# Optimization experiments

Hardware: AMD Instinct MI355X
Metric: run time of the kernel (lower is better)

## Reference

```python
import jax, jax.numpy as jnp
import numpy as np

HDIM = 1024
N_CLASSES = 50257
CUTOFFS = [2000, 10000, N_CLASSES]  # shortlist=2000, clusters: [2000,10000), [10000,50257)
DIV = 4.0
HEAD_SIZE = CUTOFFS[0] + 2  # shortlist + 2 cluster logits


def setup_inputs() -> dict:
    key = jax.random.key(0)
    ks = jax.random.split(key, 12)
    B, S, K = 8, 512, 256
    N = B * K
    hsz0 = int(HDIM // (DIV ** 1))  # 256
    hsz1 = int(HDIM // (DIV ** 2))  # 64
    osz0 = CUTOFFS[1] - CUTOFFS[0]  # 8000
    osz1 = CUTOFFS[2] - CUTOFFS[1]  # 40257
    w = 0.02
    return {
        "targets": jax.random.randint(ks[0], (N,), 0, N_CLASSES),
        "last_hidden_states": jax.random.normal(ks[1], (B, S, HDIM), dtype=jnp.float32),
        "cls_tokens_batch": jax.random.normal(ks[2], (B, HDIM), dtype=jnp.float32),
        "idx": jax.random.randint(ks[3], (B, K), 0, S),
        "head_W": jax.random.normal(ks[4], (HEAD_SIZE, HDIM), dtype=jnp.float32) * w,
        "head_b": jnp.zeros((HEAD_SIZE,), dtype=jnp.float32),
        "proj0_W": jax.random.normal(ks[5], (hsz0, HDIM), dtype=jnp.float32) * w,
        "out0_W": jax.random.normal(ks[6], (osz0, hsz0), dtype=jnp.float32) * w,
        "proj1_W": jax.random.normal(ks[7], (hsz1, HDIM), dtype=jnp.float32) * w,
        "out1_W": jax.random.normal(ks[8], (osz1, hsz1), dtype=jnp.float32) * w,
    }


def reference(targets, last_hidden_states, cls_tokens_batch, idx,
              head_W, head_b, proj0_W, out0_W, proj1_W, out1_W):
    # Gather context token embeddings: [B, K, H] -> [N, H]
    B, S, H = last_hidden_states.shape
    x = last_hidden_states[jnp.arange(B)[:, None], idx].reshape(-1, H)
    N = x.shape[0]
    c0, c1 = CUTOFFS[0], CUTOFFS[1]

    # Head: shortlist logits + per-cluster routing logits, [N, c0+2]
    head_logprob = jax.nn.log_softmax(x @ head_W.T + head_b, axis=-1)
    # Tail clusters: low-rank projection then output GEMM + log-softmax
    lp0 = jax.nn.log_softmax((x @ proj0_W.T) @ out0_W.T, axis=-1)  # [N, 8000]
    lp1 = jax.nn.log_softmax((x @ proj1_W.T) @ out1_W.T, axis=-1)  # [N, 40257]

    n = jnp.arange(N)
    t = targets
    short = head_logprob[n, jnp.clip(t, 0, c0 - 1)]
    mid = head_logprob[:, c0] + lp0[n, jnp.clip(t - c0, 0, lp0.shape[1] - 1)]
    high = head_logprob[:, c0 + 1] + lp1[n, jnp.clip(t - c1, 0, lp1.shape[1] - 1)]
    out = jnp.where(t < c0, short, jnp.where(t < c1, mid, high))  # target log-probs [N]
    loss = -jnp.mean(out)
    return out, loss
```

## Files before the change

kernel.cpp:

```cpp
#include <hip/hip_runtime.h>
#include <hip/hip_bf16.h>

#define NROWS 2048
#define L2E 1.4426950408889634f

typedef float f32x4 __attribute__((ext_vector_type(4)));
typedef __bf16 bf16x8 __attribute__((ext_vector_type(8)));
typedef short s16x8 __attribute__((ext_vector_type(8)));

typedef const __attribute__((address_space(1))) unsigned int* gas_t;
typedef __attribute__((address_space(3))) unsigned int* las_t;

__device__ __forceinline__ unsigned short f2bf(float f) {
    unsigned int u = __float_as_uint(f);
    unsigned int r = (u + 0x7FFFu + ((u >> 16) & 1u)) >> 16;
    return (unsigned short)r;
}
__device__ __forceinline__ float bf2f(unsigned short u) {
    return __uint_as_float((unsigned int)u << 16);
}
__device__ __forceinline__ f32x4 mfma16(s16x8 a, s16x8 b, f32x4 c) {
    return __builtin_amdgcn_mfma_f32_16x16x32_bf16(
        __builtin_bit_cast(bf16x8, a), __builtin_bit_cast(bf16x8, b), c, 0, 0, 0);
}

__global__ void k_prologue(const float* __restrict__ lhs, const int* __restrict__ idx,
                           const float* __restrict__ hw, const float* __restrict__ p0w,
                           const float* __restrict__ p1w, const float* __restrict__ o0w,
                           const float* __restrict__ o1w, const float* __restrict__ hb,
                           const int* __restrict__ tgt,
                           unsigned short* __restrict__ xb, unsigned short* __restrict__ hWb,
                           unsigned short* __restrict__ pW01, unsigned short* __restrict__ o0Wb,
                           unsigned short* __restrict__ o1Wb,
                           float* __restrict__ bias_s, int* __restrict__ tc,
                           unsigned long long* __restrict__ lossacc,
                           unsigned int* __restrict__ ticket) {
    int bid = blockIdx.x;
    if (bid < 2048) {
        int tid = bid * 256 + threadIdx.x;
        int n = tid >> 8;
        int c = (tid & 255) << 2;
        int b = n >> 8, k = n & 255;
        int srow = idx[(b << 8) + k];
        const float4 v = *reinterpret_cast<const float4*>(
            lhs + (((size_t)b << 9) + srow) * 1024 + c);
        ushort4 o = make_ushort4(f2bf(v.x), f2bf(v.y), f2bf(v.z), f2bf(v.w));
        *reinterpret_cast<ushort4*>(xb + (size_t)n * 1024 + c) = o;
        return;
    }
    bid -= 2048;
    if (bid < 6968) {
        const long B0 = 2048L * 1024;
        const long B1 = B0 + 384L * 1024;
        const long B2 = B1 + 8064L * 256;
        const long B3 = B2 + 40320L * 64;
        long e = ((long)bid * 256 + threadIdx.x) * 4;
        if (e >= B3) return;
        const float* src; unsigned short* dst; long rows; int colshift; long base;
        float sc;
        if (e < B0)      { base = 0;  src = hw;  dst = hWb;  rows = 2002;  colshift = 10; sc = L2E; }
        else if (e < B1) {
            long l = e - B0;
            long row = l >> 10;
            unsigned short* d = pW01 + l;
            ushort4 o;
            if (row < 256) {
                float4 v = *reinterpret_cast<const float4*>(p0w + l);
                o = make_ushort4(f2bf(v.x), f2bf(v.y), f2bf(v.z), f2bf(v.w));
            } else if (row < 320) {
                float4 v = *reinterpret_cast<const float4*>(p1w + (l - 256L * 1024));
                o = make_ushort4(f2bf(v.x), f2bf(v.y), f2bf(v.z), f2bf(v.w));
            } else {
                o = make_ushort4(0, 0, 0, 0);
            }
            *reinterpret_cast<ushort4*>(d) = o;
            return;
        }
        else if (e < B2) { base = B1; src = o0w; dst = o0Wb; rows = 8000;  colshift = 8; sc = L2E; }
        else             { base = B2; src = o1w; dst = o1Wb; rows = 40257; colshift = 6; sc = L2E; }
        long l = e - base;
        long row = l >> colshift;
        ushort4 o;
        if (row < rows) {
            float4 v = *reinterpret_cast<const float4*>(src + l);
            o = make_ushort4(f2bf(v.x * sc), f2bf(v.y * sc), f2bf(v.z * sc), f2bf(v.w * sc));
        } else {
            o = make_ushort4(0, 0, 0, 0);
        }
        *reinterpret_cast<ushort4*>(dst + l) = o;
        return;
    }
    bid -= 6968;
    int n = bid * 256 + threadIdx.x;
    if (n >= 2048) return;
    if (n == 0) { *lossacc = 0ull; *ticket = 0u; }
    bias_s[n] = (n < 2002) ? hb[n] * L2E : -1e30f;
    int t = tgt[n];
    tc[n] = min(t, 1999);
    tc[2048 + n] = min(max(t - 2000, 0), 7999);
    tc[4096 + n] = min(max(t - 10000, 0), 40256);
}

template <int NT>
__global__ __launch_bounds__(256)
void k_mm(const unsigned short* __restrict__ A, int lda,
          const unsigned short* __restrict__ B, int ldb,
          const float* __restrict__ bias, float* __restrict__ partial,
          unsigned short* __restrict__ hout, int hstride, int hcols, int fsplit) {
    __shared__ unsigned short As[2][64 * 64];
    __shared__ unsigned short Bs[2][128 * 64];
    const int tid = threadIdx.x;
    const int lane = tid & 63, wid = tid >> 6;
    const int wc = wid;
    const int g = lane >> 4, cl = lane & 15;
    const int row0 = blockIdx.x * 64;
    const int col0 = blockIdx.y * 128;

    const int sr = wid * 8 + (lane >> 3);
    const int swz = ((lane & 7) ^ (lane >> 3)) * 8;
    const unsigned short* Ab = A + (size_t)(row0 + sr) * lda + swz;
    const unsigned short* Bb = B + (size_t)(col0 + sr) * ldb + swz;

    auto stage = [&](int buf, int kt) {
        unsigned short* la = &As[buf][wid * 8 * 64];
        unsigned short* lb = &Bs[buf][wid * 8 * 64];
#pragma unroll
        for (int i = 0; i < 2; ++i)
            __builtin_amdgcn_global_load_lds((gas_t)(const void*)(Ab + kt + (size_t)i * 32 * lda),
                                             (las_t)(void*)(la + i * 32 * 64), 16, 0, 0);
#pragma unroll
        for (int i = 0; i < 4; ++i)
            __builtin_amdgcn_global_load_lds((gas_t)(const void*)(Bb + kt + (size_t)i * 32 * ldb),
                                             (las_t)(void*)(lb + i * 32 * 64), 16, 0, 0);
    };

    f32x4 acc[4][2] = {};
    stage(0, 0);
    asm volatile("s_waitcnt vmcnt(0)" ::: "memory");
    __builtin_amdgcn_s_barrier();
    const int sA = (cl & 7);
    for (int t = 0; t < NT; ++t) {
        if (t + 1 < NT) stage((t + 1) & 1, (t + 1) * 64);
        const unsigned short* Al = &As[t & 1][cl * 64];
        const unsigned short* Bl = &Bs[t & 1][(wc * 32 + cl) * 64];
#pragma unroll
        for (int kk2 = 0; kk2 < 2; ++kk2) {
            const int slot = ((kk2 * 4 + g) ^ sA) * 8;
            s16x8 a[4], b[2];
#pragma unroll
            for (int mi = 0; mi < 4; ++mi)
                a[mi] = *reinterpret_cast<const s16x8*>(Al + mi * 16 * 64 + slot);
#pragma unroll
            for (int ni = 0; ni < 2; ++ni)
                b[ni] = *reinterpret_cast<const s16x8*>(Bl + ni * 16 * 64 + slot);
#pragma unroll
            for (int mi = 0; mi < 4; ++mi)
#pragma unroll
                for (int ni = 0; ni < 2; ++ni)
                    acc[mi][ni] = mfma16(a[mi], b[ni], acc[mi][ni]);
        }
        if (t + 1 < NT) {
            asm volatile("s_waitcnt vmcnt(0)" ::: "memory");
            __builtin_amdgcn_s_barrier();
        }
    }

    if ((int)blockIdx.y >= fsplit) {
        int c0 = col0 - fsplit * 128;
#pragma unroll
        for (int mi = 0; mi < 4; ++mi)
#pragma unroll
            for (int ni = 0; ni < 2; ++ni) {
                int col = c0 + wc * 32 + ni * 16 + cl;
                if (col < hcols) {
#pragma unroll
                    for (int r = 0; r < 4; ++r) {
                        int row = row0 + mi * 16 + g * 4 + r;
                        hout[(size_t)row * hstride + col] = f2bf(acc[mi][ni][r]);
                    }
                }
            }
    } else {
        float bv0 = bias[col0 + wc * 32 + cl];
        float bv1 = bias[col0 + wc * 32 + 16 + cl];
        int strip = blockIdx.y * 4 + wc;
#pragma unroll
        for (int mi = 0; mi < 4; ++mi)
#pragma unroll
            for (int r = 0; r < 4; ++r) {
                float s = __builtin_amdgcn_exp2f(acc[mi][0][r] + bv0)
                        + __builtin_amdgcn_exp2f(acc[mi][1][r] + bv1);
                s += __shfl_xor(s, 1, 64);
                s += __shfl_xor(s, 2, 64);
                s += __shfl_xor(s, 4, 64);
                s += __shfl_xor(s, 8, 64);
                if (cl == 0)
                    partial[(size_t)strip * NROWS + row0 + mi * 16 + g * 4 + r] = s;
            }
    }
}

#define OUT1_IT 5
__global__ __launch_bounds__(256)
void k_tail(const unsigned short* __restrict__ h01, const unsigned short* __restrict__ o0Wb,
            const unsigned short* __restrict__ o1Wb, const unsigned short* __restrict__ xb,
            const float* __restrict__ headW, const float* __restrict__ hb,
            const float* __restrict__ o0w, const float* __restrict__ o1w,
            const int* __restrict__ tc,
            float* __restrict__ p0, float* __restrict__ p1,
            float* __restrict__ tgh, float* __restrict__ r0, float* __restrict__ r1,
            float* __restrict__ tg0, float* __restrict__ tg1) {
    __shared__ unsigned short smem[4][128 * 64];
    const int tid = threadIdx.x;
    const int lane = tid & 63, wid = tid >> 6;
    const int wr = wid >> 1, wc = wid & 1;
    const int g = lane >> 4, cl = lane & 15;
    int bid = ((int)blockIdx.x & 7) * 316 + ((int)blockIdx.x >> 3);

    if (bid < 1008) {
        const int row0 = (bid & 15) * 128;
        const int col0 = (bid >> 4) * 128;
        const int sr = wid * 8 + (lane >> 3);
        const int swz = ((lane & 7) ^ (lane >> 3)) * 8;
        const unsigned short* Ab = h01 + (size_t)(row0 + sr) * 320 + swz;
        const unsigned short* Bb = o0Wb + (size_t)(col0 + sr) * 256 + swz;
        auto stage = [&](int buf, int kt) {
            unsigned short* la = &smem[buf][wid * 8 * 64];
            unsigned short* lb = &smem[2 + buf][wid * 8 * 64];
#pragma unroll
            for (int i = 0; i < 4; ++i) {
                __builtin_amdgcn_global_load_lds((gas_t)(const void*)(Ab + kt + (size_t)i * 32 * 320),
                                                 (las_t)(void*)(la + i * 32 * 64), 16, 0, 0);
                __builtin_amdgcn_global_load_lds((gas_t)(const void*)(Bb + kt + (size_t)i * 32 * 256),
                                                 (las_t)(void*)(lb + i * 32 * 64), 16, 0, 0);
            }
        };
        f32x4 acc[4][4] = {};
        stage(0, 0);
        asm volatile("s_waitcnt vmcnt(0)" ::: "memory");
        __builtin_amdgcn_s_barrier();
        const int sA = (cl & 7);
        for (int t = 0; t < 4; ++t) {
            if (t < 3) stage((t + 1) & 1, (t + 1) * 64);
            const unsigned short* Al = &smem[t & 1][(wr * 64 + cl) * 64];
            const unsigned short* Bl = &smem[2 + (t & 1)][(wc * 64 + cl) * 64];
#pragma unroll
            for (int kk2 = 0; kk2 < 2; ++kk2) {
                const int slot = ((kk2 * 4 + g) ^ sA) * 8;
                s16x8 a[4], b[4];
#pragma unroll
                for (int mi = 0; mi < 4; ++mi)
                    a[mi] = *reinterpret_cast<const s16x8*>(Al + mi * 16 * 64 + slot);
#pragma unroll
                for (int ni = 0; ni < 4; ++ni)
                    b[ni] = *reinterpret_cast<const s16x8*>(Bl + ni * 16 * 64 + slot);
#pragma unroll
                for (int mi = 0; mi < 4; ++mi)
#pragma unroll
                    for (int ni = 0; ni < 4; ++ni)
                        acc[mi][ni] = mfma16(a[mi], b[ni], acc[mi][ni]);
            }
            if (t < 3) {
                asm volatile("s_waitcnt vmcnt(0)" ::: "memory");
                __builtin_amdgcn_s_barrier();
            }
        }
        int strip = (bid >> 4) * 2 + wc;
#pragma unroll
        for (int mi = 0; mi < 4; ++mi)
#pragma unroll
            for (int r = 0; r < 4; ++r) {
                float s = 0.f;
#pragma unroll
                for (int ni = 0; ni < 4; ++ni)
                    s += __builtin_amdgcn_exp2f(acc[mi][ni][r]);
                s += __shfl_xor(s, 1, 64);
                s += __shfl_xor(s, 2, 64);
                s += __shfl_xor(s, 4, 64);
                s += __shfl_xor(s, 8, 64);
                if (cl == 0)
                    p0[(size_t)strip * NROWS + row0 + wr * 64 + mi * 16 + g * 4 + r] = s;
            }
        return;
    }
    if (bid < 2016) {
        bid -= 1008;
        const int row0 = (bid & 15) * 128 + wr * 64;
        const int yb = bid >> 4;
        const int t0 = yb * OUT1_IT;
        s16x8 a[4][2];
#pragma unroll
        for (int mi = 0; mi < 4; ++mi)
#pragma unroll
            for (int kk = 0; kk < 2; ++kk)
                a[mi][kk] = *reinterpret_cast<const s16x8*>(
                    h01 + (size_t)(row0 + mi * 16 + cl) * 320 + 256 + kk * 32 + g * 8);
        const int sr = wid * 8 + (lane >> 3);
        const int swz = ((lane & 7) ^ (lane >> 3)) * 8;
        auto stage = [&](int buf, int tile) {
            const unsigned short* gb = o1Wb + ((size_t)tile * 128 + sr) * 64 + swz;
            unsigned short* lb = &smem[buf][wid * 8 * 64];
#pragma unroll
            for (int i = 0; i < 4; ++i)
                __builtin_amdgcn_global_load_lds((gas_t)(const void*)(gb + (size_t)i * 32 * 64),
                                                 (las_t)(void*)(lb + i * 32 * 64), 16, 0, 0);
        };
        float sexp[4][4] = {};
        const f32x4 z4 = {0.f, 0.f, 0.f, 0.f};
        stage(0, t0);
        asm volatile("s_waitcnt vmcnt(0)" ::: "memory");
        __builtin_amdgcn_s_barrier();
        int buf = 0;
        const int sA = (cl & 7);
#pragma unroll 1
        for (int it = 0; it < OUT1_IT; ++it) {
            if (it + 1 < OUT1_IT) stage(buf ^ 1, t0 + it + 1);
            const unsigned short* Bl = smem[buf];
#pragma unroll
            for (int ni = 0; ni < 4; ++ni) {
                const unsigned short* br = Bl + (wc * 64 + ni * 16 + cl) * 64;
                s16x8 b0 = *reinterpret_cast<const s16x8*>(br + (g ^ sA) * 8);
                s16x8 b1 = *reinterpret_cast<const s16x8*>(br + ((4 + g) ^ sA) * 8);
                f32x4 acc[4];
#pragma unroll
                for (int mi = 0; mi < 4; ++mi)
                    acc[mi] = mfma16(a[mi][0], b0, z4);
#pragma unroll
                for (int mi = 0; mi < 4; ++mi)
                    acc[mi] = mfma16(a[mi][1], b1, acc[mi]);
#pragma unroll
                for (int mi = 0; mi < 4; ++mi)
#pragma unroll
                    for (int r = 0; r < 4; ++r)
                        sexp[mi][r] += __builtin_amdgcn_exp2f(acc[mi][r]);
            }
            if (it + 1 < OUT1_IT) {
                asm volatile("s_waitcnt vmcnt(0)" ::: "memory");
                __builtin_amdgcn_s_barrier();
                buf ^= 1;
            }
        }
#pragma unroll
        for (int mi = 0; mi < 4; ++mi)
#pragma unroll
            for (int r = 0; r < 4; ++r) {
                float s = sexp[mi][r];
                s += __shfl_xor(s, 1, 64);
                s += __shfl_xor(s, 2, 64);
                s += __shfl_xor(s, 4, 64);
                s += __shfl_xor(s, 8, 64);
                if (cl == 0)
                    p1[(size_t)(yb * 2 + wc) * NROWS + row0 + mi * 16 + g * 4 + r] = s;
            }
        return;
    }
    bid -= 2016;
    int n = (bid * 256 + tid) >> 6;
    int tch = tc[n], tc0 = tc[2048 + n], tc1 = tc[4096 + n];
    const unsigned short* xr = xb + (size_t)n * 1024 + lane * 16;
    s16x8 x0 = *reinterpret_cast<const s16x8*>(xr);
    s16x8 x1 = *reinterpret_cast<const s16x8*>(xr + 8);
    const float* wh = headW + (size_t)tch * 1024 + lane * 16;
    const float* wa = headW + (size_t)2000 * 1024 + lane * 16;
    const float* wb = headW + (size_t)2001 * 1024 + lane * 16;
    float dh = 0.f, da = 0.f, db = 0.f;
#pragma unroll
    for (int i = 0; i < 8; ++i) {
        float xv = bf2f((unsigned short)x0[i]);
        dh += xv * wh[i]; da += xv * wa[i]; db += xv * wb[i];
    }
#pragma unroll
    for (int i = 0; i < 8; ++i) {
        float xv = bf2f((unsigned short)x1[i]);
        dh += xv * wh[8 + i]; da += xv * wa[8 + i]; db += xv * wb[8 + i];
    }
    ushort4 h0v = *reinterpret_cast<const ushort4*>(h01 + (size_t)n * 320 + lane * 4);
    float4 w0v = *reinterpret_cast<const float4*>(o0w + (size_t)tc0 * 256 + lane * 4);
    float d2 = bf2f(h0v.x) * w0v.x + bf2f(h0v.y) * w0v.y +
               bf2f(h0v.z) * w0v.z + bf2f(h0v.w) * w0v.w;
    float d3 = bf2f(h01[(size_t)n * 320 + 256 + lane]) * o1w[(size_t)tc1 * 64 + lane];
#pragma unroll
    for (int m = 1; m < 64; m <<= 1) {
        dh += __shfl_xor(dh, m, 64);
        da += __shfl_xor(da, m, 64);
        db += __shfl_xor(db, m, 64);
        d2 += __shfl_xor(d2, m, 64);
        d3 += __shfl_xor(d3, m, 64);
    }
    if (lane == 0) {
        tgh[n] = dh + hb[tch];
        r0[n] = da + hb[2000];
        r1[n] = db + hb[2001];
        tg0[n] = d2;
        tg1[n] = d3;
    }
}

__global__ void k_finalize(const float* __restrict__ ph, const float* __restrict__ p0,
                           const float* __restrict__ p1, const float* __restrict__ tgh,
                           const float* __restrict__ r0, const float* __restrict__ r1,
                           const float* __restrict__ tg0, const float* __restrict__ tg1,
                           const int* __restrict__ tgt, float* __restrict__ outv,
                           unsigned long long* __restrict__ lossacc,
                           unsigned int* __restrict__ ticket) {
    int n = blockIdx.x * 128 + threadIdx.x;
    float sh = 0.f, s0 = 0.f, s1 = 0.f;
    for (int s = 0; s < 64; ++s) sh += ph[(size_t)s * NROWS + n];
    for (int s = 0; s < 126; ++s) s0 += p0[(size_t)s * NROWS + n];
    for (int s = 0; s < 126; ++s) s1 += p1[(size_t)s * NROWS + n];
    s0 -= 64.f;
    s1 -= 63.f;
    float lh = __logf(sh), l0 = __logf(s0), l1 = __logf(s1);
    int t = tgt[n];
    float o;
    if (t < 2000) o = tgh[n] - lh;
    else if (t < 10000) o = (r0[n] - lh) + (tg0[n] - l0);
    else o = (r1[n] - lh) + (tg1[n] - l1);
    outv[n] = o;
    __shared__ float red[128];
    red[threadIdx.x] = o;
    __syncthreads();
    for (int s = 64; s > 0; s >>= 1) {
        if (threadIdx.x < s) red[threadIdx.x] += red[threadIdx.x + s];
        __syncthreads();
    }
    if (threadIdx.x == 0) {
        long long fx = __double2ll_rn((double)red[0] * 1048576.0);
        atomicAdd(lossacc, (unsigned long long)fx);
        __threadfence();
        unsigned int tk = atomicAdd(ticket, 1u);
        if (tk == 15u) {
            unsigned long long v = atomicAdd(lossacc, 0ull);
            outv[NROWS] = (float)(-((double)(long long)v / 1048576.0) / 2048.0);
        }
    }
}

extern "C" void kernel_launch(void* const* d_in, const int* in_sizes, int n_in,
                              void* d_out, int out_size, void* d_ws, size_t ws_size,
                              hipStream_t stream) {
    const int* targets   = (const int*)d_in[0];
    const float* lhs     = (const float*)d_in[1];
    const int* idx       = (const int*)d_in[3];
    const float* head_W  = (const float*)d_in[4];
    const float* head_b  = (const float*)d_in[5];
    const float* proj0_W = (const float*)d_in[6];
    const float* out0_W  = (const float*)d_in[7];
    const float* proj1_W = (const float*)d_in[8];
    const float* out1_W  = (const float*)d_in[9];

    char* ws = (char*)d_ws;
    size_t off = 0;
    auto alloc = [&](size_t bytes) -> void* {
        void* p = ws + off;
        off += (bytes + 255) & ~(size_t)255;
        return p;
    };

    unsigned short* xb   = (unsigned short*)alloc((size_t)2048 * 1024 * 2);
    unsigned short* wB   = (unsigned short*)alloc((size_t)2432 * 1024 * 2);
    unsigned short* hWb  = wB;
    unsigned short* pW01 = wB + (size_t)2048 * 1024;
    unsigned short* o0Wb = (unsigned short*)alloc((size_t)8064 * 256 * 2);
    unsigned short* o1Wb = (unsigned short*)alloc((size_t)40320 * 64 * 2);
    unsigned short* h01  = (unsigned short*)alloc((size_t)2048 * 320 * 2);
    float* ph  = (float*)alloc((size_t)64 * 2048 * 4);
    float* p0  = (float*)alloc((size_t)126 * 2048 * 4);
    float* p1  = (float*)alloc((size_t)126 * 2048 * 4);
    float* tgh = (float*)alloc(2048 * 4);
    float* r0  = (float*)alloc(2048 * 4);
    float* r1  = (float*)alloc(2048 * 4);
    float* tg0 = (float*)alloc(2048 * 4);
    float* tg1 = (float*)alloc(2048 * 4);
    int*   tc  = (int*)alloc(3 * 2048 * 4);
    float* bias_s = (float*)alloc(2048 * 4);
    unsigned long long* lossacc = (unsigned long long*)alloc(8);
    unsigned int* ticket = (unsigned int*)alloc(4);

    k_prologue<<<9024, 256, 0, stream>>>(lhs, idx, head_W, proj0_W, proj1_W, out0_W, out1_W,
                                         head_b, targets,
                                         xb, hWb, pW01, o0Wb, o1Wb, bias_s, tc,
                                         lossacc, ticket);

    k_mm<16><<<dim3(32, 19), 256, 0, stream>>>(
        xb, 1024, wB, 1024, bias_s, ph, h01, 320, 320, 16);

    k_tail<<<2528, 256, 0, stream>>>(h01, o0Wb, o1Wb, xb, head_W, head_b, out0_W, out1_W,
                                     tc, p0, p1, tgh, r0, r1, tg0, tg1);

    float* outv = (float*)d_out;
    k_finalize<<<16, 128, 0, stream>>>(ph, p0, p1, tgh, r0, r1, tg0, tg1, targets,
                                       outv, lossacc, ticket);
}
```

Before: 95.66 us.

## Split projection GEMM out and merge head GEMM into tail kernel

The previous combined GEMM launch computed both the head logits partial sums (16 column tiles) and the low-rank projections (3 tiles) in one 608-block grid, so the tail kernel had to wait for the whole head GEMM. Now a small 96-block kernel computes only the projections, and the head GEMM's exp-sum epilogue moves into the big tail kernel as 512 extra blocks. The head work can then run alongside the out0/out1 tail GEMMs instead of sitting on the critical path. Block ID remapping with stride-8 swizzles is added per section, likely aimed at XCD/L2 locality. The trade-off is that the tiny projection launch underuses the GPU.

After: 91.05 us. 1.05x faster.

```diff
diff --git a/kernel.cpp b/kernel.cpp
--- a/kernel.cpp
+++ b/kernel.cpp
@@ -101,36 +101,35 @@
     tc[4096 + n] = min(max(t - 10000, 0), 40256);
 }
 
-template <int NT>
 __global__ __launch_bounds__(256)
-void k_mm(const unsigned short* __restrict__ A, int lda,
-          const unsigned short* __restrict__ B, int ldb,
-          const float* __restrict__ bias, float* __restrict__ partial,
-          unsigned short* __restrict__ hout, int hstride, int hcols, int fsplit) {
+void k_proj(const unsigned short* __restrict__ A, const unsigned short* __restrict__ B,
+            unsigned short* __restrict__ hout) {
     __shared__ unsigned short As[2][64 * 64];
     __shared__ unsigned short Bs[2][128 * 64];
     const int tid = threadIdx.x;
     const int lane = tid & 63, wid = tid >> 6;
     const int wc = wid;
     const int g = lane >> 4, cl = lane & 15;
-    const int row0 = blockIdx.x * 64;
-    const int col0 = blockIdx.y * 128;
+    int raw = (int)blockIdx.x;
+    int bid = (raw & 7) * 12 + (raw >> 3);
+    const int row0 = (bid & 31) * 64;
+    const int col0 = (bid >> 5) * 128;
 
     const int sr = wid * 8 + (lane >> 3);
     const int swz = ((lane & 7) ^ (lane >> 3)) * 8;
-    const unsigned short* Ab = A + (size_t)(row0 + sr) * lda + swz;
-    const unsigned short* Bb = B + (size_t)(col0 + sr) * ldb + swz;
+    const unsigned short* Ab = A + (size_t)(row0 + sr) * 1024 + swz;
+    const unsigned short* Bb = B + (size_t)(col0 + sr) * 1024 + swz;
 
     auto stage = [&](int buf, int kt) {
         unsigned short* la = &As[buf][wid * 8 * 64];
         unsigned short* lb = &Bs[buf][wid * 8 * 64];
 #pragma unroll
         for (int i = 0; i < 2; ++i)
-            __builtin_amdgcn_global_load_lds((gas_t)(const void*)(Ab + kt + (size_t)i * 32 * lda),
+            __builtin_amdgcn_global_load_lds((gas_t)(const void*)(Ab + kt + (size_t)i * 32 * 1024),
                                              (las_t)(void*)(la + i * 32 * 64), 16, 0, 0);
 #pragma unroll
         for (int i = 0; i < 4; ++i)
-            __builtin_amdgcn_global_load_lds((gas_t)(const void*)(Bb + kt + (size_t)i * 32 * ldb),
+            __builtin_amdgcn_global_load_lds((gas_t)(const void*)(Bb + kt + (size_t)i * 32 * 1024),
                                              (las_t)(void*)(lb + i * 32 * 64), 16, 0, 0);
     };
 
@@ -139,8 +138,8 @@
     asm volatile("s_waitcnt vmcnt(0)" ::: "memory");
     __builtin_amdgcn_s_barrier();
     const int sA = (cl & 7);
-    for (int t = 0; t < NT; ++t) {
-        if (t + 1 < NT) stage((t + 1) & 1, (t + 1) * 64);
+    for (int t = 0; t < 16; ++t) {
+        if (t + 1 < 16) stage((t + 1) & 1, (t + 1) * 64);
         const unsigned short* Al = &As[t & 1][cl * 64];
         const unsigned short* Bl = &Bs[t & 1][(wc * 32 + cl) * 64];
 #pragma unroll
@@ -159,31 +158,97 @@
                 for (int ni = 0; ni < 2; ++ni)
                     acc[mi][ni] = mfma16(a[mi], b[ni], acc[mi][ni]);
         }
-        if (t + 1 < NT) {
+        if (t + 1 < 16) {
             asm volatile("s_waitcnt vmcnt(0)" ::: "memory");
             __builtin_amdgcn_s_barrier();
         }
     }
-
-    if ((int)blockIdx.y >= fsplit) {
-        int c0 = col0 - fsplit * 128;
-#pragma unroll
-        for (int mi = 0; mi < 4; ++mi)
-#pragma unroll
-            for (int ni = 0; ni < 2; ++ni) {
-                int col = c0 + wc * 32 + ni * 16 + cl;
-                if (col < hcols) {
-#pragma unroll
-                    for (int r = 0; r < 4; ++r) {
-                        int row = row0 + mi * 16 + g * 4 + r;
-                        hout[(size_t)row * hstride + col] = f2bf(acc[mi][ni][r]);
-                    }
+#pragma unroll
+    for (int mi = 0; mi < 4; ++mi)
+#pragma unroll
+        for (int ni = 0; ni < 2; ++ni) {
+            int col = col0 + wc * 32 + ni * 16 + cl;
+            if (col < 320) {
+#pragma unroll
+                for (int r = 0; r < 4; ++r) {
+                    int row = row0 + mi * 16 + g * 4 + r;
+                    hout[(size_t)row * 320 + col] = f2bf(acc[mi][ni][r]);
                 }
             }
-    } else {
-        float bv0 = bias[col0 + wc * 32 + cl];
-        float bv1 = bias[col0 + wc * 32 + 16 + cl];
-        int strip = blockIdx.y * 4 + wc;
+        }
+}
+
+#define OUT1_IT 5
+__global__ __launch_bounds__(256)
+void k_bigtail(const unsigned short* __restrict__ xb, const unsigned short* __restrict__ hWb,
+               const unsigned short* __restrict__ h01, const unsigned short* __restrict__ o0Wb,
+               const unsigned short* __restrict__ o1Wb,
+               const float* __restrict__ headW, const float* __restrict__ hb,
+               const float* __restrict__ o0w, const float* __restrict__ o1w,
+               const float* __restrict__ bias_s, const int* __restrict__ tc,
+               float* __restrict__ ph, float* __restrict__ p0, float* __restrict__ p1,
+               float* __restrict__ tgh, float* __restrict__ r0, float* __restrict__ r1,
+               float* __restrict__ tg0, float* __restrict__ tg1) {
+    __shared__ unsigned short smem[4][128 * 64];
+    const int tid = threadIdx.x;
+    const int lane = tid & 63, wid = tid >> 6;
+    const int g = lane >> 4, cl = lane & 15;
+    int raw = (int)blockIdx.x;
+
+    if (raw < 512) {
+        int bid = (raw & 7) * 64 + (raw >> 3);
+        const int wc = wid;
+        const int row0 = (bid & 31) * 64;
+        const int col0 = (bid >> 5) * 128;
+        const int sr = wid * 8 + (lane >> 3);
+        const int swz = ((lane & 7) ^ (lane >> 3)) * 8;
+        const unsigned short* Ab = xb + (size_t)(row0 + sr) * 1024 + swz;
+        const unsigned short* Bb = hWb + (size_t)(col0 + sr) * 1024 + swz;
+        auto stage = [&](int buf, int kt) {
+            unsigned short* la = &smem[2 + buf][wid * 8 * 64];
+            unsigned short* lb = &smem[buf][wid * 8 * 64];
+#pragma unroll
+            for (int i = 0; i < 2; ++i)
+                __builtin_amdgcn_global_load_lds((gas_t)(const void*)(Ab + kt + (size_t)i * 32 * 1024),
+                                                 (las_t)(void*)(la + i * 32 * 64), 16, 0, 0);
+#pragma unroll
+            for (int i = 0; i < 4; ++i)
+                __builtin_amdgcn_global_load_lds((gas_t)(const void*)(Bb + kt + (size_t)i * 32 * 1024),
+                                                 (las_t)(void*)(lb + i * 32 * 64), 16, 0, 0);
+        };
+        f32x4 acc[4][2] = {};
+        stage(0, 0);
+        asm volatile("s_waitcnt vmcnt(0)" ::: "memory");
+        __builtin_amdgcn_s_barrier();
+        const int sA = (cl & 7);
+        for (int t = 0; t < 16; ++t) {
+            if (t + 1 < 16) stage((t + 1) & 1, (t + 1) * 64);
+            const unsigned short* Al = &smem[2 + (t & 1)][cl * 64];
+            const unsigned short* Bl = &smem[t & 1][(wc * 32 + cl) * 64];
+#pragma unroll
+            for (int kk2 = 0; kk2 < 2; ++kk2) {
+                const int slot = ((kk2 * 4 + g) ^ sA) * 8;
+                s16x8 a[4], b[2];
+#pragma unroll
+                for (int mi = 0; mi < 4; ++mi)
+                    a[mi] = *reinterpret_cast<const s16x8*>(Al + mi * 16 * 64 + slot);
+#pragma unroll
+                for (int ni = 0; ni < 2; ++ni)
+                    b[ni] = *reinterpret_cast<const s16x8*>(Bl + ni * 16 * 64 + slot);
+#pragma unroll
+                for (int mi = 0; mi < 4; ++mi)
+#pragma unroll
+                    for (int ni = 0; ni < 2; ++ni)
+                        acc[mi][ni] = mfma16(a[mi], b[ni], acc[mi][ni]);
+            }
+            if (t + 1 < 16) {
+                asm volatile("s_waitcnt vmcnt(0)" ::: "memory");
+                __builtin_amdgcn_s_barrier();
+            }
+        }
+        float bv0 = bias_s[col0 + wc * 32 + cl];
+        float bv1 = bias_s[col0 + wc * 32 + 16 + cl];
+        int strip = (bid >> 5) * 4 + wc;
 #pragma unroll
         for (int mi = 0; mi < 4; ++mi)
 #pragma unroll
@@ -195,96 +260,14 @@
                 s += __shfl_xor(s, 4, 64);
                 s += __shfl_xor(s, 8, 64);
                 if (cl == 0)
-                    partial[(size_t)strip * NROWS + row0 + mi * 16 + g * 4 + r] = s;
-            }
-    }
-}
-
-#define OUT1_IT 5
-__global__ __launch_bounds__(256)
-void k_tail(const unsigned short* __restrict__ h01, const unsigned short* __restrict__ o0Wb,
-            const unsigned short* __restrict__ o1Wb, const unsigned short* __restrict__ xb,
-            const float* __restrict__ headW, const float* __restrict__ hb,
-            const float* __restrict__ o0w, const float* __restrict__ o1w,
-            const int* __restrict__ tc,
-            float* __restrict__ p0, float* __restrict__ p1,
-            float* __restrict__ tgh, float* __restrict__ r0, float* __restrict__ r1,
-            float* __restrict__ tg0, float* __restrict__ tg1) {
-    __shared__ unsigned short smem[4][128 * 64];
-    const int tid = threadIdx.x;
-    const int lane = tid & 63, wid = tid >> 6;
-    const int wr = wid >> 1, wc = wid & 1;
-    const int g = lane >> 4, cl = lane & 15;
-    int bid = ((int)blockIdx.x & 7) * 316 + ((int)blockIdx.x >> 3);
-
-    if (bid < 1008) {
-        const int row0 = (bid & 15) * 128;
-        const int col0 = (bid >> 4) * 128;
-        const int sr = wid * 8 + (lane >> 3);
-        const int swz = ((lane & 7) ^ (lane >> 3)) * 8;
-        const unsigned short* Ab = h01 + (size_t)(row0 + sr) * 320 + swz;
-        const unsigned short* Bb = o0Wb + (size_t)(col0 + sr) * 256 + swz;
-        auto stage = [&](int buf, int kt) {
-            unsigned short* la = &smem[buf][wid * 8 * 64];
-            unsigned short* lb = &smem[2 + buf][wid * 8 * 64];
-#pragma unroll
-            for (int i = 0; i < 4; ++i) {
-                __builtin_amdgcn_global_load_lds((gas_t)(const void*)(Ab + kt + (size_t)i * 32 * 320),
-                                                 (las_t)(void*)(la + i * 32 * 64), 16, 0, 0);
-                __builtin_amdgcn_global_load_lds((gas_t)(const void*)(Bb + kt + (size_t)i * 32 * 256),
-                                                 (las_t)(void*)(lb + i * 32 * 64), 16, 0, 0);
-            }
-        };
-        f32x4 acc[4][4] = {};
-        stage(0, 0);
-        asm volatile("s_waitcnt vmcnt(0)" ::: "memory");
-        __builtin_amdgcn_s_barrier();
-        const int sA = (cl & 7);
-        for (int t = 0; t < 4; ++t) {
-            if (t < 3) stage((t + 1) & 1, (t + 1) * 64);
-            const unsigned short* Al = &smem[t & 1][(wr * 64 + cl) * 64];
-            const unsigned short* Bl = &smem[2 + (t & 1)][(wc * 64 + cl) * 64];
-#pragma unroll
-            for (int kk2 = 0; kk2 < 2; ++kk2) {
-                const int slot = ((kk2 * 4 + g) ^ sA) * 8;
-                s16x8 a[4], b[4];
-#pragma unroll
-                for (int mi = 0; mi < 4; ++mi)
-                    a[mi] = *reinterpret_cast<const s16x8*>(Al + mi * 16 * 64 + slot);
-#pragma unroll
-                for (int ni = 0; ni < 4; ++ni)
-                    b[ni] = *reinterpret_cast<const s16x8*>(Bl + ni * 16 * 64 + slot);
-#pragma unroll
-                for (int mi = 0; mi < 4; ++mi)
-#pragma unroll
-                    for (int ni = 0; ni < 4; ++ni)
-                        acc[mi][ni] = mfma16(a[mi], b[ni], acc[mi][ni]);
-            }
-            if (t < 3) {
-                asm volatile("s_waitcnt vmcnt(0)" ::: "memory");
-                __builtin_amdgcn_s_barrier();
-            }
-        }
-        int strip = (bid >> 4) * 2 + wc;
-#pragma unroll
-        for (int mi = 0; mi < 4; ++mi)
-#pragma unroll
-            for (int r = 0; r < 4; ++r) {
-                float s = 0.f;
-#pragma unroll
-                for (int ni = 0; ni < 4; ++ni)
-                    s += __builtin_amdgcn_exp2f(acc[mi][ni][r]);
-                s += __shfl_xor(s, 1, 64);
-                s += __shfl_xor(s, 2, 64);
-                s += __shfl_xor(s, 4, 64);
-                s += __shfl_xor(s, 8, 64);
-                if (cl == 0)
-                    p0[(size_t)strip * NROWS + row0 + wr * 64 + mi * 16 + g * 4 + r] = s;
+                    ph[(size_t)strip * NROWS + row0 + mi * 16 + g * 4 + r] = s;
             }
         return;
     }
-    if (bid < 2016) {
-        bid -= 1008;
+    if (raw < 1520) {
+        int b2 = raw - 512;
+        int bid = (b2 & 7) * 126 + (b2 >> 3);
+        const int wr = wid >> 1, wc = wid & 1;
         const int row0 = (bid & 15) * 128 + wr * 64;
         const int yb = bid >> 4;
         const int t0 = yb * OUT1_IT;
@@ -354,7 +337,77 @@
             }
         return;
     }
-    bid -= 2016;
+    if (raw < 2528) {
+        int b2 = raw - 1520;
+        int bid = (b2 & 7) * 126 + (b2 >> 3);
+        const int wr = wid >> 1, wc = wid & 1;
+        const int row0 = (bid & 15) * 128;
+        const int col0 = (bid >> 4) * 128;
+        const int sr = wid * 8 + (lane >> 3);
+        const int swz = ((lane & 7) ^ (lane >> 3)) * 8;
+        const unsigned short* Ab = h01 + (size_t)(row0 + sr) * 320 + swz;
+        const unsigned short* Bb = o0Wb + (size_t)(col0 + sr) * 256 + swz;
+        auto stage = [&](int buf, int kt) {
+            unsigned short* la = &smem[2 + buf][wid * 8 * 64];
+            unsigned short* lb = &smem[buf][wid * 8 * 64];
+#pragma unroll
+            for (int i = 0; i < 4; ++i) {
+                __builtin_amdgcn_global_load_lds((gas_t)(const void*)(Ab + kt + (size_t)i * 32 * 320),
+                                                 (las_t)(void*)(la + i * 32 * 64), 16, 0, 0);
+                __builtin_amdgcn_global_load_lds((gas_t)(const void*)(Bb + kt + (size_t)i * 32 * 256),
+                                                 (las_t)(void*)(lb + i * 32 * 64), 16, 0, 0);
+            }
+        };
+        f32x4 acc[4][4] = {};
+        stage(0, 0);
+        asm volatile("s_waitcnt vmcnt(0)" ::: "memory");
+        __builtin_amdgcn_s_barrier();
+        const int sA = (cl & 7);
+        for (int t = 0; t < 4; ++t) {
+            if (t < 3) stage((t + 1) & 1, (t + 1) * 64);
+            const unsigned short* Al = &smem[2 + (t & 1)][(wr * 64 + cl) * 64];
+            const unsigned short* Bl = &smem[t & 1][(wc * 64 + cl) * 64];
+#pragma unroll
+            for (int kk2 = 0; kk2 < 2; ++kk2) {
+                const int slot = ((kk2 * 4 + g) ^ sA) * 8;
+                s16x8 a[4], b[4];
+#pragma unroll
+                for (int mi = 0; mi < 4; ++mi)
+                    a[mi] = *reinterpret_cast<const s16x8*>(Al + mi * 16 * 64 + slot);
+#pragma unroll
+                for (int ni = 0; ni < 4; ++ni)
+                    b[ni] = *reinterpret_cast<const s16x8*>(Bl + ni * 16 * 64 + slot);
+#pragma unroll
+                for (int mi = 0; mi < 4; ++mi)
+#pragma unroll
+                    for (int ni = 0; ni < 4; ++ni)
+                        acc[mi][ni] = mfma16(a[mi], b[ni], acc[mi][ni]);
+            }
+            if (t < 3) {
+                asm volatile("s_waitcnt vmcnt(0)" ::: "memory");
+                __builtin_amdgcn_s_barrier();
+            }
+        }
+        int strip = (bid >> 4) * 2 + wc;
+#pragma unroll
+        for (int mi = 0; mi < 4; ++mi)
+#pragma unroll
+            for (int r = 0; r < 4; ++r) {
+                float s = 0.f;
+#pragma unroll
+                for (int ni = 0; ni < 4; ++ni)
+                    s += __builtin_amdgcn_exp2f(acc[mi][ni][r]);
+                s += __shfl_xor(s, 1, 64);
+                s += __shfl_xor(s, 2, 64);
+                s += __shfl_xor(s, 4, 64);
+                s += __shfl_xor(s, 8, 64);
+                if (cl == 0)
+                    p0[(size_t)strip * NROWS + row0 + wr * 64 + mi * 16 + g * 4 + r] = s;
+            }
+        return;
+    }
+    int b3 = raw - 2528;
+    int bid = (b3 & 7) * 64 + (b3 >> 3);
     int n = (bid * 256 + tid) >> 6;
     int tch = tc[n], tc0 = tc[2048 + n], tc1 = tc[4096 + n];
     const unsigned short* xr = xb + (size_t)n * 1024 + lane * 16;
@@ -482,11 +535,11 @@
                                          xb, hWb, pW01, o0Wb, o1Wb, bias_s, tc,
                                          lossacc, ticket);
 
-    k_mm<16><<<dim3(32, 19), 256, 0, stream>>>(
-        xb, 1024, wB, 1024, bias_s, ph, h01, 320, 320, 16);
-
-    k_tail<<<2528, 256, 0, stream>>>(h01, o0Wb, o1Wb, xb, head_W, head_b, out0_W, out1_W,
-                                     tc, p0, p1, tgh, r0, r1, tg0, tg1);
+    k_proj<<<96, 256, 0, stream>>>(xb, pW01, h01);
+
+    k_bigtail<<<3040, 256, 0, stream>>>(xb, hWb, h01, o0Wb, o1Wb, head_W, head_b,
+                                        out0_W, out1_W, bias_s, tc,
+                                        ph, p0, p1, tgh, r0, r1, tg0, tg1);
 
     float* outv = (float*)d_out;
     k_finalize<<<16, 128, 0, stream>>>(ph, p0, p1, tgh, r0, r1, tg0, tg1, targets,
```
